# Kernel tuning notes

Measured on AMD Instinct MI355X. Metric: run time of the kernel, lower is better.

## Reference

```python
import jax, jax.numpy as jnp
import numpy as np

BS, SEQ_Q = 16, 2048
ATTN_DIM, K_DIM, HEAD, RANK = 1024, 1024, 16, 16
A_H = ATTN_DIM // HEAD        # 64
K_R = K_DIM // RANK           # 64
HR = HEAD * RANK              # 256
EXP = 2
EPS = 1e-5


def setup_inputs() -> dict:
    key = jax.random.key(0)
    ks = jax.random.split(key, 12)
    n = lambda k, shape, scale=1.0: jax.random.normal(k, shape, dtype=jnp.float32) * scale
    lin = ATTN_DIM ** -0.5
    xav = (2.0 / (K_R + RANK)) ** 0.5  # xavier_normal for factor
    return {
        "Q": n(ks[0], (BS, SEQ_Q, ATTN_DIM)),
        "K": n(ks[1], (BS, K_DIM, ATTN_DIM)),
        "V": n(ks[2], (BS, K_DIM, ATTN_DIM)),
        "WQ": n(ks[3], (ATTN_DIM, ATTN_DIM), lin), "bQ": jnp.zeros((ATTN_DIM,), jnp.float32),
        "WK": n(ks[4], (ATTN_DIM, ATTN_DIM), lin), "bK": jnp.zeros((ATTN_DIM,), jnp.float32),
        "WV": n(ks[5], (ATTN_DIM, ATTN_DIM), lin), "bV": jnp.zeros((ATTN_DIM,), jnp.float32),
        "factor": n(ks[6], (1, A_H, K_R, RANK), xav),
        "W1": n(ks[7], (EXP * ATTN_DIM, ATTN_DIM), lin), "b1": jnp.zeros((EXP * ATTN_DIM,), jnp.float32),
        "W2": n(ks[8], (ATTN_DIM, EXP * ATTN_DIM), (EXP * ATTN_DIM) ** -0.5), "b2": jnp.zeros((ATTN_DIM,), jnp.float32),
        "gamma": jnp.ones((ATTN_DIM,), jnp.float32),
        "beta": jnp.zeros((ATTN_DIM,), jnp.float32),
    }


def reference(Q, K, V, WQ, bQ, WK, bK, WV, bV, factor, W1, b1, W2, b2, gamma, beta):
    bs = Q.shape[0]
    fac = factor[0]  # [a_h, k_r, rank]
    # Q path: [bs, a_h, head*rank, seq_q/rank]
    q = (Q @ WQ.T + bQ).reshape(bs, A_H, HR, -1)
    # K/V path: low-rank projection via learned factor -> [bs, a_h, head*rank, rank]
    k = jnp.einsum('bahk,akr->bahr', (K @ WK.T + bK).reshape(bs, A_H, HR, K_R), fac)
    v = jnp.einsum('bahk,akr->bahr', (V @ WV.T + bV).reshape(bs, A_H, HR, K_R), fac)
    # scores: Q^T K / sqrt(head*rank) -> [bs, a_h, L, rank]
    scores = jnp.einsum('bahl,bahr->balr', q, k) / jnp.float32(HR) ** 0.5
    attn = jax.nn.softmax(scores, axis=-1)
    # attn @ V^T -> [bs, a_h, L, head*rank], then flatten back to [bs, seq_q, attn_dim]
    ctx = jnp.einsum('balr,bahr->balh', attn, v).reshape(bs, -1, ATTN_DIM)
    # FFN (dropout = identity in eval)
    h = jax.nn.relu(ctx @ W1.T + b1)
    y = h @ W2.T + b2
    # residual + LayerNorm
    x = y + Q
    mu = jnp.mean(x, axis=-1, keepdims=True)
    var = jnp.var(x, axis=-1, keepdims=True)
    return (x - mu) * jax.lax.rsqrt(var + EPS) * gamma + beta
```

## Files before the change

### kernel.cpp

```cpp
#include <hip/hip_runtime.h>
#include <cstdint>

typedef unsigned short u16;
typedef unsigned int   u32;
typedef u16    u16x4  __attribute__((ext_vector_type(4)));
typedef u16    u16x8  __attribute__((ext_vector_type(8)));
typedef __bf16 bf16x8 __attribute__((ext_vector_type(8)));
typedef float  f32x4  __attribute__((ext_vector_type(4)));

__device__ __forceinline__ u16 f2b(float x) {
  u32 u = __builtin_bit_cast(u32, x);
  u32 r = (u + 0x7fffu + ((u >> 16) & 1u)) >> 16;
  return (u16)r;
}
__device__ __forceinline__ float b2f(u16 u) {
  return __builtin_bit_cast(float, (u32)u << 16);
}

__device__ __forceinline__ void gl2lds16(const u16* g, u16* l) {
  __builtin_amdgcn_global_load_lds(
      (__attribute__((address_space(1))) void*)g,
      (__attribute__((address_space(3))) void*)l, 16, 0, 0);
}

struct CvtArgs {
  const float* src[8];
  u16*         dst[8];
  long         end[8];
};

__global__ __launch_bounds__(256) void cvt_all(CvtArgs a)
{
  long g = (long)blockIdx.x * 1024;
  int seg = 0;
#pragma unroll
  for (int s = 0; s < 8; ++s) seg += (g >= a.end[s]) ? 1 : 0;
  long base = (seg == 0) ? 0 : a.end[seg - 1];
  long off = g - base + (long)threadIdx.x * 4;
  const float* src = a.src[seg];
  u16* dst = a.dst[seg];
  f32x4 v = *(const f32x4*)&src[off];
  u16x4 o = { f2b(v[0]), f2b(v[1]), f2b(v[2]), f2b(v[3]) };
  *(u16x4*)&dst[off] = o;
}

#define BM 128
#define BN 128
#define BK 64

__global__ __launch_bounds__(256) void gemm_bt(
    const u16* __restrict__ A, const u16* __restrict__ B,
    const float* __restrict__ bias, u16* __restrict__ C,
    int M, int N, int K, int relu)
{
  __shared__ __attribute__((aligned(16))) u16 As[BM * BK];
  __shared__ __attribute__((aligned(16))) u16 Bs[BN * BK];

  const int tid  = threadIdx.x;
  const int lane = tid & 63;
  const int wave = tid >> 6;
  const int lr   = lane & 15;
  const int quad = lane >> 4;
  const int wm = (wave >> 1) * 64;
  const int wn = (wave & 1) * 64;

  const int Nb = gridDim.x;
  const int flat = blockIdx.y * Nb + blockIdx.x;
  const int sg  = flat / (8 * Nb);
  const int rem = flat - sg * 8 * Nb;
  const int bx  = rem >> 3;
  const int by  = sg * 8 + (rem & 7);

  const long m0 = (long)by * BM;
  const long n0 = (long)bx * BN;

  long goff[4];
#pragma unroll
  for (int c = 0; c < 4; ++c) {
    const int p = tid + 256 * c;
    const int row = p >> 3;
    const int logcol = (p & 7) ^ (row & 7);
    goff[c] = (long)row * K + logcol * 8;
  }

  const u16* Ab = A + m0 * K;
  const u16* Bb = B + n0 * K;

  const int ph0 = quad ^ (lane & 7);
  const int ph1 = (quad + 4) ^ (lane & 7);

  f32x4 acc[4][4] = {};

  for (int k0 = 0; k0 < K; k0 += BK) {
    __syncthreads();
#pragma unroll
    for (int c = 0; c < 4; ++c) {
      gl2lds16(Ab + goff[c] + k0, &As[(tid + 256 * c) * 8]);
      gl2lds16(Bb + goff[c] + k0, &Bs[(tid + 256 * c) * 8]);
    }
    __syncthreads();

#pragma unroll
    for (int kh = 0; kh < 2; ++kh) {
      const int ph = kh ? ph1 : ph0;
      bf16x8 af[4], bff[4];
#pragma unroll
      for (int i = 0; i < 4; ++i)
        af[i] = *(const bf16x8*)&As[(wm + i * 16 + lr) * BK + ph * 8];
#pragma unroll
      for (int i = 0; i < 4; ++i)
        bff[i] = *(const bf16x8*)&Bs[(wn + i * 16 + lr) * BK + ph * 8];
#pragma unroll
      for (int i = 0; i < 4; ++i)
#pragma unroll
        for (int j = 0; j < 4; ++j)
          acc[i][j] = __builtin_amdgcn_mfma_f32_16x16x32_bf16(af[i], bff[j], acc[i][j], 0, 0, 0);
    }
  }

#pragma unroll
  for (int j = 0; j < 4; ++j) {
    const int col = wn + j * 16 + lr;
    const float bv = bias[n0 + col];
#pragma unroll
    for (int i = 0; i < 4; ++i) {
#pragma unroll
      for (int r = 0; r < 4; ++r) {
        const int row = wm + i * 16 + quad * 4 + r;
        float v = acc[i][j][r] + bv;
        if (relu) v = fmaxf(v, 0.0f);
        C[(m0 + row) * (long)N + (n0 + col)] = f2b(v);
      }
    }
  }
}

__global__ __launch_bounds__(256) void attn_kernel(
    const u16* __restrict__ Qp, const u16* __restrict__ Kp,
    const u16* __restrict__ Vp, const float* __restrict__ factor,
    u16* __restrict__ Ctx)
{
  __shared__ __attribute__((aligned(16))) float fac_s[64 * 16];
  __shared__ __attribute__((aligned(16))) float k_s[256][20];
  __shared__ __attribute__((aligned(16))) float v_s[256][20];
  __shared__ __attribute__((aligned(16))) float s_s[128][20];

  const int t = threadIdx.x;
  const int b = blockIdx.x >> 6;
  const int a = blockIdx.x & 63;

  for (int i = t; i < 1024; i += 256) fac_s[i] = factor[a * 1024 + i];
  __syncthreads();

  {
    const long kb = (((long)(b * 1024 + a * 16)) << 10) + (long)t * 64;
    float kacc[16] = {}, vacc[16] = {};
    for (int kk8 = 0; kk8 < 64; kk8 += 8) {
      u16x8 kv8 = *(const u16x8*)&Kp[kb + kk8];
      u16x8 vv8 = *(const u16x8*)&Vp[kb + kk8];
#pragma unroll
      for (int j = 0; j < 8; ++j) {
        const float kv = b2f(kv8[j]), vv = b2f(vv8[j]);
        const float* fr = &fac_s[(kk8 + j) * 16];
#pragma unroll
        for (int r = 0; r < 16; ++r) { kacc[r] += kv * fr[r]; vacc[r] += vv * fr[r]; }
      }
    }
#pragma unroll
    for (int r = 0; r < 16; ++r) { k_s[t][r] = kacc[r] * 0.0625f; v_s[t][r] = vacc[r]; }
  }
  __syncthreads();

  {
    const int l = t & 127, half = t >> 7;
    const long qb = (((long)(b * 2048 + a * 32)) << 10) + l;
    f32x4 acc0 = {}, acc1 = {};
    for (int h = 0; h < 256; ++h) {
      const float qv = b2f(Qp[qb + (long)h * 128]);
      f32x4 k0 = *(const f32x4*)&k_s[h][half * 8];
      f32x4 k1 = *(const f32x4*)&k_s[h][half * 8 + 4];
      acc0 += k0 * qv;
      acc1 += k1 * qv;
    }
    *(f32x4*)&s_s[l][half * 8]     = acc0;
    *(f32x4*)&s_s[l][half * 8 + 4] = acc1;
  }
  __syncthreads();

  if (t < 128) {
    float vals[16];
    float m = -1e30f;
#pragma unroll
    for (int r = 0; r < 16; ++r) { vals[r] = s_s[t][r]; m = fmaxf(m, vals[r]); }
    float sum = 0.0f;
#pragma unroll
    for (int r = 0; r < 16; ++r) { vals[r] = __expf(vals[r] - m); sum += vals[r]; }
    const float inv = 1.0f / sum;
#pragma unroll
    for (int r = 0; r < 16; ++r) s_s[t][r] = vals[r] * inv;
  }
  __syncthreads();

  {
    f32x4 v0 = *(const f32x4*)&v_s[t][0];
    f32x4 v1 = *(const f32x4*)&v_s[t][4];
    f32x4 v2 = *(const f32x4*)&v_s[t][8];
    f32x4 v3 = *(const f32x4*)&v_s[t][12];
    const long cb = (((long)(b * 2048 + a * 32)) << 10) + t;
    for (int l = 0; l < 128; ++l) {
      f32x4 a0 = *(const f32x4*)&s_s[l][0];
      f32x4 a1 = *(const f32x4*)&s_s[l][4];
      f32x4 a2 = *(const f32x4*)&s_s[l][8];
      f32x4 a3 = *(const f32x4*)&s_s[l][12];
      f32x4 p = a0 * v0 + a1 * v1 + a2 * v2 + a3 * v3;
      Ctx[cb + (long)l * 256] = f2b(p[0] + p[1] + p[2] + p[3]);
    }
  }
}

__global__ __launch_bounds__(256) void ln_kernel(
    const u16* __restrict__ Y, const float* __restrict__ Qin,
    const float* __restrict__ gamma, const float* __restrict__ beta,
    float* __restrict__ out)
{
  const long row = blockIdx.x;
  const int t = threadIdx.x;
  const long base = (row << 10) + (long)t * 4;

  u16x4 y4 = *(const u16x4*)&Y[base];
  f32x4 q4 = *(const f32x4*)&Qin[base];
  f32x4 x;
#pragma unroll
  for (int c = 0; c < 4; ++c) x[c] = b2f(y4[c]) + q4[c];

  float s  = x[0] + x[1] + x[2] + x[3];
  float sq = x[0]*x[0] + x[1]*x[1] + x[2]*x[2] + x[3]*x[3];
#pragma unroll
  for (int o = 1; o < 64; o <<= 1) {
    s  += __shfl_xor(s, o);
    sq += __shfl_xor(sq, o);
  }
  __shared__ float red[8];
  if ((t & 63) == 0) { red[(t >> 6) * 2] = s; red[(t >> 6) * 2 + 1] = sq; }
  __syncthreads();
  s  = red[0] + red[2] + red[4] + red[6];
  sq = red[1] + red[3] + red[5] + red[7];

  const float mean = s * (1.0f / 1024.0f);
  const float var  = sq * (1.0f / 1024.0f) - mean * mean;
  const float rstd = rsqrtf(var + 1e-5f);

  f32x4 g4 = *(const f32x4*)&gamma[t * 4];
  f32x4 be4 = *(const f32x4*)&beta[t * 4];
  f32x4 o4;
#pragma unroll
  for (int c = 0; c < 4; ++c) o4[c] = (x[c] - mean) * rstd * g4[c] + be4[c];
  *(f32x4*)&out[base] = o4;
}

extern "C" void kernel_launch(void* const* d_in, const int* in_sizes, int n_in,
                              void* d_out, int out_size, void* d_ws, size_t ws_size,
                              hipStream_t stream)
{
  (void)in_sizes; (void)n_in; (void)out_size; (void)ws_size;
  const float* Q      = (const float*)d_in[0];
  const float* K      = (const float*)d_in[1];
  const float* V      = (const float*)d_in[2];
  const float* WQ     = (const float*)d_in[3];
  const float* bQ     = (const float*)d_in[4];
  const float* WK     = (const float*)d_in[5];
  const float* bK     = (const float*)d_in[6];
  const float* WV     = (const float*)d_in[7];
  const float* bV     = (const float*)d_in[8];
  const float* factor = (const float*)d_in[9];
  const float* W1     = (const float*)d_in[10];
  const float* b1     = (const float*)d_in[11];
  const float* W2     = (const float*)d_in[12];
  const float* b2     = (const float*)d_in[13];
  const float* gamma  = (const float*)d_in[14];
  const float* beta   = (const float*)d_in[15];
  float* out = (float*)d_out;

  const long NQ = 33554432L;
  const long NK = 16777216L;
  const long ND = 1048576L;
  const long NW = 2097152L;

  char* w = (char*)d_ws;
  u16* Qb  = (u16*)(w);
  u16* Kb  = (u16*)(w + 67108864L);
  u16* Vb  = (u16*)(w + 100663296L);
  u16* WQb = (u16*)(w + 134217728L);
  u16* WKb = (u16*)(w + 136314880L);
  u16* WVb = (u16*)(w + 138412032L);
  u16* W1b = (u16*)(w + 140509184L);
  u16* W2b = (u16*)(w + 144703488L);
  u16* Qp  = (u16*)(w + 148897792L);
  u16* Kp  = (u16*)(w + 216006656L);
  u16* Vp  = (u16*)(w + 249561088L);
  u16* Ctx = (u16*)(w + 283115520L);
  u16* Hb  = (u16*)(w);
  u16* Yb  = (u16*)(w + 216006656L);

  CvtArgs ca;
  ca.src[0] = Q;  ca.dst[0] = Qb;
  ca.src[1] = K;  ca.dst[1] = Kb;
  ca.src[2] = V;  ca.dst[2] = Vb;
  ca.src[3] = WQ; ca.dst[3] = WQb;
  ca.src[4] = WK; ca.dst[4] = WKb;
  ca.src[5] = WV; ca.dst[5] = WVb;
  ca.src[6] = W1; ca.dst[6] = W1b;
  ca.src[7] = W2; ca.dst[7] = W2b;
  long sizes[8] = { NQ, NK, NK, ND, ND, ND, NW, NW };
  long cum = 0;
  for (int i = 0; i < 8; ++i) { cum += sizes[i]; ca.end[i] = cum; }
  cvt_all<<<(int)(cum / 1024), 256, 0, stream>>>(ca);

  gemm_bt<<<dim3(8, 256),  256, 0, stream>>>(Qb, WQb, bQ, Qp, 32768, 1024, 1024, 0);
  gemm_bt<<<dim3(8, 128),  256, 0, stream>>>(Kb, WKb, bK, Kp, 16384, 1024, 1024, 0);
  gemm_bt<<<dim3(8, 128),  256, 0, stream>>>(Vb, WVb, bV, Vp, 16384, 1024, 1024, 0);

  attn_kernel<<<1024, 256, 0, stream>>>(Qp, Kp, Vp, factor, Ctx);

  gemm_bt<<<dim3(16, 256), 256, 0, stream>>>(Ctx, W1b, b1, Hb, 32768, 2048, 1024, 1);
  gemm_bt<<<dim3(8, 256),  256, 0, stream>>>(Hb, W2b, b2, Yb, 32768, 1024, 2048, 0);

  ln_kernel<<<32768, 256, 0, stream>>>(Yb, Q, gamma, beta, out);
}
```

Baseline: 1.041 ms.

## Replace 128x128 GEMM with 256x256 double-buffered pipelined 8-wave GEMM

Replaces the 128x128 single-buffered bf16 GEMM with a 256x256-tile, 512-thread kernel. It double-buffers LDS and interleaves global-to-LDS staging of the next K tile with the MFMA phases of the current one, using explicit barriers, waitcnts and setprio. The larger tile raises arithmetic intensity and the pipeline hides global load latency. In exchange it uses 128KB of LDS per block and many accumulator registers, which limits occupancy, and the hand-tuned waitcnt counts are fragile.

```diff
diff --git a/kernel.cpp b/kernel.cpp
--- a/kernel.cpp
+++ b/kernel.cpp
@@ -7,6 +7,8 @@
 typedef u16    u16x8  __attribute__((ext_vector_type(8)));
 typedef __bf16 bf16x8 __attribute__((ext_vector_type(8)));
 typedef float  f32x4  __attribute__((ext_vector_type(4)));
+
+template<int N> struct IC { static constexpr int v = N; };
 
 __device__ __forceinline__ u16 f2b(float x) {
   u32 u = __builtin_bit_cast(u32, x);
@@ -44,25 +46,21 @@
   *(u16x4*)&dst[off] = o;
 }
 
-#define BM 128
-#define BN 128
-#define BK 64
-
-__global__ __launch_bounds__(256) void gemm_bt(
+__global__ __launch_bounds__(512, 2) void gemm256(
     const u16* __restrict__ A, const u16* __restrict__ B,
     const float* __restrict__ bias, u16* __restrict__ C,
     int M, int N, int K, int relu)
 {
-  __shared__ __attribute__((aligned(16))) u16 As[BM * BK];
-  __shared__ __attribute__((aligned(16))) u16 Bs[BN * BK];
+  __shared__ __attribute__((aligned(16))) u16 Abuf[2][16384];
+  __shared__ __attribute__((aligned(16))) u16 Bbuf[2][16384];
 
   const int tid  = threadIdx.x;
   const int lane = tid & 63;
   const int wave = tid >> 6;
   const int lr   = lane & 15;
   const int quad = lane >> 4;
-  const int wm = (wave >> 1) * 64;
-  const int wn = (wave & 1) * 64;
+  const int wr   = wave >> 2;
+  const int wc   = wave & 3;
 
   const int Nb = gridDim.x;
   const int flat = blockIdx.y * Nb + blockIdx.x;
@@ -70,63 +68,143 @@
   const int rem = flat - sg * 8 * Nb;
   const int bx  = rem >> 3;
   const int by  = sg * 8 + (rem & 7);
-
-  const long m0 = (long)by * BM;
-  const long n0 = (long)bx * BN;
-
-  long goff[4];
-#pragma unroll
-  for (int c = 0; c < 4; ++c) {
-    const int p = tid + 256 * c;
+  const long m0 = (long)by * 256;
+  const long n0 = (long)bx * 256;
+
+  long goff[2]; int loff[2];
+#pragma unroll
+  for (int c = 0; c < 2; ++c) {
+    const int p = tid + 512 * c;
     const int row = p >> 3;
     const int logcol = (p & 7) ^ (row & 7);
     goff[c] = (long)row * K + logcol * 8;
-  }
-
-  const u16* Ab = A + m0 * K;
-  const u16* Bb = B + n0 * K;
-
-  const int ph0 = quad ^ (lane & 7);
-  const int ph1 = (quad + 4) ^ (lane & 7);
-
-  f32x4 acc[4][4] = {};
-
-  for (int k0 = 0; k0 < K; k0 += BK) {
-    __syncthreads();
-#pragma unroll
-    for (int c = 0; c < 4; ++c) {
-      gl2lds16(Ab + goff[c] + k0, &As[(tid + 256 * c) * 8]);
-      gl2lds16(Bb + goff[c] + k0, &Bs[(tid + 256 * c) * 8]);
-    }
-    __syncthreads();
-
-#pragma unroll
-    for (int kh = 0; kh < 2; ++kh) {
-      const int ph = kh ? ph1 : ph0;
-      bf16x8 af[4], bff[4];
-#pragma unroll
-      for (int i = 0; i < 4; ++i)
-        af[i] = *(const bf16x8*)&As[(wm + i * 16 + lr) * BK + ph * 8];
-#pragma unroll
-      for (int i = 0; i < 4; ++i)
-        bff[i] = *(const bf16x8*)&Bs[(wn + i * 16 + lr) * BK + ph * 8];
-#pragma unroll
-      for (int i = 0; i < 4; ++i)
-#pragma unroll
-        for (int j = 0; j < 4; ++j)
-          acc[i][j] = __builtin_amdgcn_mfma_f32_16x16x32_bf16(af[i], bff[j], acc[i][j], 0, 0, 0);
-    }
+    loff[c] = p * 8;
+  }
+
+  const u16* Ag = A + m0 * K;
+  const u16* Bg = B + n0 * K;
+
+  const int ph_0 = quad ^ (lane & 7);
+  const int ph_1 = (quad + 4) ^ (lane & 7);
+
+  f32x4 acc[8][4] = {};
+
+  auto stage = [&](u16* lds, const u16* g, int h) {
+#pragma unroll
+    for (int c = 0; c < 2; ++c)
+      gl2lds16(g + (long)h * 128 * K + goff[c], lds + h * 8192 + loff[c]);
+  };
+  auto ldA = [&](const u16* Ac, int i, int kk) -> bf16x8 {
+    return *(const bf16x8*)&Ac[(wr * 128 + i * 16 + lr) * 64 + (kk ? ph_1 : ph_0) * 8];
+  };
+  auto ldB = [&](const u16* Bc, int j, int kk) -> bf16x8 {
+    return *(const bf16x8*)&Bc[(wc * 64 + j * 16 + lr) * 64 + (kk ? ph_1 : ph_0) * 8];
+  };
+
+  auto ktile = [&](auto sa, auto sb, auto vm, const u16* Ac, const u16* Bc,
+                   u16* Ast, u16* Bst, const u16* gAn, const u16* gBn) {
+    bf16x8 af[4][2], b0f[2][2], b1f[2][2];
+#pragma unroll
+    for (int i = 0; i < 4; ++i) { af[i][0] = ldA(Ac, i, 0); af[i][1] = ldA(Ac, i, 1); }
+#pragma unroll
+    for (int j = 0; j < 2; ++j) { b0f[j][0] = ldB(Bc, j, 0); b0f[j][1] = ldB(Bc, j, 1); }
+    if constexpr (decltype(sa)::v) stage(Ast, gAn, 0);
+    __builtin_amdgcn_s_barrier();
+    asm volatile("s_waitcnt lgkmcnt(0)" ::: "memory");
+    __builtin_amdgcn_s_setprio(1);
+#pragma unroll
+    for (int i = 0; i < 4; ++i)
+#pragma unroll
+      for (int j = 0; j < 2; ++j) {
+        acc[i][j] = __builtin_amdgcn_mfma_f32_16x16x32_bf16(af[i][0], b0f[j][0], acc[i][j], 0, 0, 0);
+        acc[i][j] = __builtin_amdgcn_mfma_f32_16x16x32_bf16(af[i][1], b0f[j][1], acc[i][j], 0, 0, 0);
+      }
+    __builtin_amdgcn_s_setprio(0);
+    __builtin_amdgcn_s_barrier();
+#pragma unroll
+    for (int j = 0; j < 2; ++j) { b1f[j][0] = ldB(Bc, 2 + j, 0); b1f[j][1] = ldB(Bc, 2 + j, 1); }
+    if constexpr (decltype(sa)::v) stage(Ast, gAn, 1);
+    __builtin_amdgcn_s_barrier();
+    asm volatile("s_waitcnt lgkmcnt(0)" ::: "memory");
+    __builtin_amdgcn_s_setprio(1);
+#pragma unroll
+    for (int i = 0; i < 4; ++i)
+#pragma unroll
+      for (int j = 0; j < 2; ++j) {
+        acc[i][2 + j] = __builtin_amdgcn_mfma_f32_16x16x32_bf16(af[i][0], b1f[j][0], acc[i][2 + j], 0, 0, 0);
+        acc[i][2 + j] = __builtin_amdgcn_mfma_f32_16x16x32_bf16(af[i][1], b1f[j][1], acc[i][2 + j], 0, 0, 0);
+      }
+    __builtin_amdgcn_s_setprio(0);
+    __builtin_amdgcn_s_barrier();
+#pragma unroll
+    for (int i = 0; i < 4; ++i) { af[i][0] = ldA(Ac, 4 + i, 0); af[i][1] = ldA(Ac, 4 + i, 1); }
+    if constexpr (decltype(sb)::v) stage(Bst, gBn, 0);
+    __builtin_amdgcn_s_barrier();
+    asm volatile("s_waitcnt lgkmcnt(0)" ::: "memory");
+    __builtin_amdgcn_s_setprio(1);
+#pragma unroll
+    for (int i = 0; i < 4; ++i)
+#pragma unroll
+      for (int j = 0; j < 2; ++j) {
+        acc[4 + i][j] = __builtin_amdgcn_mfma_f32_16x16x32_bf16(af[i][0], b0f[j][0], acc[4 + i][j], 0, 0, 0);
+        acc[4 + i][j] = __builtin_amdgcn_mfma_f32_16x16x32_bf16(af[i][1], b0f[j][1], acc[4 + i][j], 0, 0, 0);
+      }
+    __builtin_amdgcn_s_setprio(0);
+    __builtin_amdgcn_s_barrier();
+    if constexpr (decltype(sb)::v) stage(Bst, gBn, 1);
+    __builtin_amdgcn_s_barrier();
+    __builtin_amdgcn_s_setprio(1);
+#pragma unroll
+    for (int i = 0; i < 4; ++i)
+#pragma unroll
+      for (int j = 0; j < 2; ++j) {
+        acc[4 + i][2 + j] = __builtin_amdgcn_mfma_f32_16x16x32_bf16(af[i][0], b1f[j][0], acc[4 + i][2 + j], 0, 0, 0);
+        acc[4 + i][2 + j] = __builtin_amdgcn_mfma_f32_16x16x32_bf16(af[i][1], b1f[j][1], acc[4 + i][2 + j], 0, 0, 0);
+      }
+    __builtin_amdgcn_s_setprio(0);
+    if constexpr (decltype(vm)::v == 4) asm volatile("s_waitcnt vmcnt(4)" ::: "memory");
+    if constexpr (decltype(vm)::v == 0) asm volatile("s_waitcnt vmcnt(0)" ::: "memory");
+    __builtin_amdgcn_s_barrier();
+  };
+
+  const int NT = K >> 6;
+
+  stage(&Abuf[0][0], Ag, 0); stage(&Abuf[0][0], Ag, 1);
+  stage(&Bbuf[0][0], Bg, 0); stage(&Bbuf[0][0], Bg, 1);
+  stage(&Bbuf[1][0], Bg + 64, 0); stage(&Bbuf[1][0], Bg + 64, 1);
+  asm volatile("s_waitcnt vmcnt(4)" ::: "memory");
+  __builtin_amdgcn_s_barrier();
+
+  for (int t = 0; t < NT - 2; ++t) {
+    const int cur = t & 1, nxt = cur ^ 1;
+    ktile(IC<1>{}, IC<1>{}, IC<4>{},
+          &Abuf[cur][0], &Bbuf[cur][0],
+          &Abuf[nxt][0], &Bbuf[cur][0],
+          Ag + (long)(t + 1) * 64, Bg + (long)(t + 2) * 64);
+  }
+  {
+    const int cur = (NT - 2) & 1, nxt = cur ^ 1;
+    ktile(IC<1>{}, IC<0>{}, IC<0>{},
+          &Abuf[cur][0], &Bbuf[cur][0],
+          &Abuf[nxt][0], nullptr,
+          Ag + (long)(NT - 1) * 64, nullptr);
+  }
+  {
+    const int cur = (NT - 1) & 1;
+    ktile(IC<0>{}, IC<0>{}, IC<-1>{},
+          &Abuf[cur][0], &Bbuf[cur][0],
+          nullptr, nullptr, nullptr, nullptr);
   }
 
 #pragma unroll
   for (int j = 0; j < 4; ++j) {
-    const int col = wn + j * 16 + lr;
+    const int col = wc * 64 + j * 16 + lr;
     const float bv = bias[n0 + col];
 #pragma unroll
-    for (int i = 0; i < 4; ++i) {
+    for (int i = 0; i < 8; ++i) {
 #pragma unroll
       for (int r = 0; r < 4; ++r) {
-        const int row = wm + i * 16 + quad * 4 + r;
+        const int row = wr * 128 + i * 16 + quad * 4 + r;
         float v = acc[i][j][r] + bv;
         if (relu) v = fmaxf(v, 0.0f);
         C[(m0 + row) * (long)N + (n0 + col)] = f2b(v);
@@ -316,14 +394,14 @@
   for (int i = 0; i < 8; ++i) { cum += sizes[i]; ca.end[i] = cum; }
   cvt_all<<<(int)(cum / 1024), 256, 0, stream>>>(ca);
 
-  gemm_bt<<<dim3(8, 256),  256, 0, stream>>>(Qb, WQb, bQ, Qp, 32768, 1024, 1024, 0);
-  gemm_bt<<<dim3(8, 128),  256, 0, stream>>>(Kb, WKb, bK, Kp, 16384, 1024, 1024, 0);
-  gemm_bt<<<dim3(8, 128),  256, 0, stream>>>(Vb, WVb, bV, Vp, 16384, 1024, 1024, 0);
+  gemm256<<<dim3(4, 128), 512, 0, stream>>>(Qb, WQb, bQ, Qp, 32768, 1024, 1024, 0);
+  gemm256<<<dim3(4, 64),  512, 0, stream>>>(Kb, WKb, bK, Kp, 16384, 1024, 1024, 0);
+  gemm256<<<dim3(4, 64),  512, 0, stream>>>(Vb, WVb, bV, Vp, 16384, 1024, 1024, 0);
 
   attn_kernel<<<1024, 256, 0, stream>>>(Qp, Kp, Vp, factor, Ctx);
 
-  gemm_bt<<<dim3(16, 256), 256, 0, stream>>>(Ctx, W1b, b1, Hb, 32768, 2048, 1024, 1);
-  gemm_bt<<<dim3(8, 256),  256, 0, stream>>>(Hb, W2b, b2, Yb, 32768, 1024, 2048, 0);
+  gemm256<<<dim3(8, 128), 512, 0, stream>>>(Ctx, W1b, b1, Hb, 32768, 2048, 1024, 1);
+  gemm256<<<dim3(4, 128), 512, 0, stream>>>(Hb, W2b, b2, Yb, 32768, 1024, 2048, 0);
 
   ln_kernel<<<32768, 256, 0, stream>>>(Yb, Q, gamma, beta, out);
 }
```

After: 979.2 us. 5.9% less time.
